# Kernel tuning notes

Measured on AMD Instinct MI355X. Metric: run time of the kernel, lower is better.

## Reference

```python
import jax, jax.numpy as jnp
import numpy as np

N_NODES = 50000


def gcn_conv(x, src, dst, W, b, n_nodes):
    """PyG GCNConv: add self-loops, sym-normalize, aggregate, linear.
    x' = D^{-1/2} (A + I) D^{-1/2} X W + b
    """
    loop = jnp.arange(n_nodes, dtype=src.dtype)
    s = jnp.concatenate([src, loop])  # [E + N]
    d = jnp.concatenate([dst, loop])
    h = x @ W  # [N, out]
    deg = jax.ops.segment_sum(jnp.ones_like(d, dtype=h.dtype), d, num_segments=n_nodes)
    dinv = jnp.where(deg > 0, jax.lax.rsqrt(deg), 0.0)
    norm = dinv[s] * dinv[d]  # [E + N]
    msg = h[s] * norm[:, None]  # gather + scale (edge-level, memory bound)
    out = jax.ops.segment_sum(msg, d, num_segments=n_nodes)
    return out + b


def setup_inputs() -> dict:
    key = jax.random.key(0)
    k1, k2, k3, k4 = jax.random.split(key, 4)
    n, e, d_in, d_hid, d_out = N_NODES, 800000, 128, 128, 64
    x = jax.random.normal(k1, (n, d_in), dtype=jnp.float32)
    edge_index = jax.random.randint(k2, (2, e), 0, n, dtype=jnp.int64)
    W1 = jax.random.normal(k3, (d_in, d_hid), dtype=jnp.float32) * (1.0 / np.sqrt(d_in))
    b1 = jnp.zeros((d_hid,), dtype=jnp.float32)
    W2 = jax.random.normal(k4, (d_hid, d_out), dtype=jnp.float32) * (1.0 / np.sqrt(d_hid))
    b2 = jnp.zeros((d_out,), dtype=jnp.float32)
    return {"x": x, "edge_index": edge_index, "W1": W1, "b1": b1, "W2": W2, "b2": b2}


def reference(x, edge_index, W1, b1, W2, b2):
    src, dst = edge_index[0], edge_index[1]
    h = gcn_conv(x, src, dst, W1, b1, N_NODES)
    h = jax.nn.relu(h)
    h = gcn_conv(h, src, dst, W2, b2, N_NODES)
    # edge-wise gather + dot product -> per-edge logits [E]
    logits = jnp.sum(h[src] * h[dst], axis=-1)
    return logits
```

## Files before the change

### kernel.cpp

```cpp
#include <hip/hip_runtime.h>
#include <hip/hip_bf16.h>


__global__ void cnt_k(const int* __restrict__ dst, int* __restrict__ cnt, int E) {
    int t = blockIdx.x * blockDim.x + threadIdx.x;
    int e = t * 4;
    if (e + 4 <= E) {
        int4 d4 = *reinterpret_cast<const int4*>(dst + e);
        atomicAdd(&cnt[d4.x], 1);
        atomicAdd(&cnt[d4.y], 1);
        atomicAdd(&cnt[d4.z], 1);
        atomicAdd(&cnt[d4.w], 1);
    } else {
        for (int i = e; i < E; i++) atomicAdd(&cnt[dst[i]], 1);
    }
}

__global__ void scan1_k(const int* __restrict__ cnt, int* __restrict__ incl,
                        int* __restrict__ bsum, int N) {
    __shared__ int sh[256];
    int i = blockIdx.x * 256 + threadIdx.x;
    int v = (i < N) ? cnt[i] : 0;
    sh[threadIdx.x] = v;
    __syncthreads();
#pragma unroll
    for (int off = 1; off < 256; off <<= 1) {
        int t = (threadIdx.x >= off) ? sh[threadIdx.x - off] : 0;
        __syncthreads();
        sh[threadIdx.x] += t;
        __syncthreads();
    }
    if (i < N) incl[i] = sh[threadIdx.x];
    if (threadIdx.x == 255) bsum[blockIdx.x] = sh[255];
}

__global__ __launch_bounds__(256) void scan23_k(const int* __restrict__ cnt,
                                                const int* __restrict__ incl,
                                                const int* __restrict__ bsum,
                                                int* __restrict__ rowptr,
                                                int* __restrict__ cursor,
                                                float* __restrict__ dinv,
                                                int N, int E, int NB) {
    __shared__ int sh[256];
    __shared__ int blockOff;
    int v = (threadIdx.x < NB) ? bsum[threadIdx.x] : 0;
    sh[threadIdx.x] = v;
    __syncthreads();
#pragma unroll
    for (int off = 1; off < 256; off <<= 1) {
        int t = (threadIdx.x >= off) ? sh[threadIdx.x - off] : 0;
        __syncthreads();
        sh[threadIdx.x] += t;
        __syncthreads();
    }
    if (threadIdx.x == blockIdx.x) blockOff = sh[threadIdx.x] - v;
    __syncthreads();
    int i = blockIdx.x * 256 + threadIdx.x;
    if (i < N) {
        int c = cnt[i];
        int excl = incl[i] - c + blockOff;
        rowptr[i] = excl;
        cursor[i] = excl;
        dinv[i] = rsqrtf(1.0f + (float)c);
    }
    if (i == 0) rowptr[N] = E;
}

__global__ __launch_bounds__(256) void gemm1_fill_k(const float* __restrict__ A,
                                                    const float* __restrict__ W,
                                                    const float* __restrict__ dscale,
                                                    float* __restrict__ Out, int M,
                                                    const int* __restrict__ src,
                                                    const int* __restrict__ dst,
                                                    int* __restrict__ cursor,
                                                    int2* __restrict__ col2, int E,
                                                    int gemmBlocks) {
    constexpr int K = 128, BM = 64, BK = 16, BN = 128, TN = 8;
    __shared__ float As[BK][BM + 4];
    __shared__ float Bs[BK][BN];

    if ((int)blockIdx.x >= gemmBlocks) {
        int t = ((int)blockIdx.x - gemmBlocks) * 256 + threadIdx.x;
        int e = t * 4;
        if (e + 4 <= E) {
            int4 s4 = *reinterpret_cast<const int4*>(src + e);
            int4 d4 = *reinterpret_cast<const int4*>(dst + e);
            int p0 = atomicAdd(&cursor[d4.x], 1);
            col2[p0] = make_int2(s4.x, e + 0);
            int p1 = atomicAdd(&cursor[d4.y], 1);
            col2[p1] = make_int2(s4.y, e + 1);
            int p2 = atomicAdd(&cursor[d4.z], 1);
            col2[p2] = make_int2(s4.z, e + 2);
            int p3 = atomicAdd(&cursor[d4.w], 1);
            col2[p3] = make_int2(s4.w, e + 3);
        } else {
            for (int i = e; i < E; i++) {
                int pos = atomicAdd(&cursor[dst[i]], 1);
                col2[pos] = make_int2(src[i], i);
            }
        }
        return;
    }

    const int tid = threadIdx.x;
    const int tx = tid & 15, ty = tid >> 4;
    const int row0 = blockIdx.x * BM;

    float acc[4][TN];
#pragma unroll
    for (int m = 0; m < 4; m++)
#pragma unroll
        for (int j = 0; j < TN; j++) acc[m][j] = 0.0f;

    const int ar = tid >> 2;
    const int ak = (tid & 3) * 4;

    for (int kt = 0; kt < K; kt += BK) {
        float4 av = make_float4(0.f, 0.f, 0.f, 0.f);
        int grow = row0 + ar;
        if (grow < M)
            av = *reinterpret_cast<const float4*>(A + (size_t)grow * K + kt + ak);
        As[ak + 0][ar] = av.x; As[ak + 1][ar] = av.y;
        As[ak + 2][ar] = av.z; As[ak + 3][ar] = av.w;

#pragma unroll
        for (int b = 0; b < 2; b++) {
            int f = b * 256 + tid;
            int brow = (f * 4) / BN;
            int bcol = (f * 4) % BN;
            float4 bv = *reinterpret_cast<const float4*>(W + (size_t)(kt + brow) * BN + bcol);
            *reinterpret_cast<float4*>(&Bs[brow][bcol]) = bv;
        }
        __syncthreads();

#pragma unroll
        for (int k = 0; k < BK; k++) {
            float4 a4 = *reinterpret_cast<const float4*>(&As[k][ty * 4]);
            float a[4] = {a4.x, a4.y, a4.z, a4.w};
            float bb[TN];
#pragma unroll
            for (int j4 = 0; j4 < TN / 4; j4++) {
                float4 b4 = *reinterpret_cast<const float4*>(&Bs[k][tx * TN + j4 * 4]);
                bb[j4 * 4 + 0] = b4.x; bb[j4 * 4 + 1] = b4.y;
                bb[j4 * 4 + 2] = b4.z; bb[j4 * 4 + 3] = b4.w;
            }
#pragma unroll
            for (int m = 0; m < 4; m++)
#pragma unroll
                for (int j = 0; j < TN; j++) acc[m][j] = fmaf(a[m], bb[j], acc[m][j]);
        }
        __syncthreads();
    }

#pragma unroll
    for (int m = 0; m < 4; m++) {
        int gr = row0 + ty * 4 + m;
        if (gr < M) {
            float dv = dscale[gr];
#pragma unroll
            for (int j4 = 0; j4 < TN / 4; j4++) {
                float4 o = make_float4(acc[m][j4 * 4 + 0] * dv, acc[m][j4 * 4 + 1] * dv,
                                       acc[m][j4 * 4 + 2] * dv, acc[m][j4 * 4 + 3] * dv);
                *reinterpret_cast<float4*>(Out + (size_t)gr * BN + tx * TN + j4 * 4) = o;
            }
        }
    }
}

__global__ __launch_bounds__(256) void gemm2_k(const float* __restrict__ A,
                                               const float* __restrict__ W,
                                               const float* __restrict__ dscale,
                                               float* __restrict__ Out, int M) {
    constexpr int K = 128, BM = 64, BK = 16, BN = 64, TN = 4;
    __shared__ float As[BK][BM + 4];
    __shared__ float Bs[BK][BN];

    const int tid = threadIdx.x;
    const int tx = tid & 15, ty = tid >> 4;
    const int row0 = blockIdx.x * BM;

    float acc[4][TN];
#pragma unroll
    for (int m = 0; m < 4; m++)
#pragma unroll
        for (int j = 0; j < TN; j++) acc[m][j] = 0.0f;

    const int ar = tid >> 2;
    const int ak = (tid & 3) * 4;

    for (int kt = 0; kt < K; kt += BK) {
        float4 av = make_float4(0.f, 0.f, 0.f, 0.f);
        int grow = row0 + ar;
        if (grow < M)
            av = *reinterpret_cast<const float4*>(A + (size_t)grow * K + kt + ak);
        av.x = fmaxf(av.x, 0.f); av.y = fmaxf(av.y, 0.f);
        av.z = fmaxf(av.z, 0.f); av.w = fmaxf(av.w, 0.f);
        As[ak + 0][ar] = av.x; As[ak + 1][ar] = av.y;
        As[ak + 2][ar] = av.z; As[ak + 3][ar] = av.w;

        {
            int f = tid;
            int brow = (f * 4) / BN;
            int bcol = (f * 4) % BN;
            float4 bv = *reinterpret_cast<const float4*>(W + (size_t)(kt + brow) * BN + bcol);
            *reinterpret_cast<float4*>(&Bs[brow][bcol]) = bv;
        }
        __syncthreads();

#pragma unroll
        for (int k = 0; k < BK; k++) {
            float4 a4 = *reinterpret_cast<const float4*>(&As[k][ty * 4]);
            float a[4] = {a4.x, a4.y, a4.z, a4.w};
            float4 b4 = *reinterpret_cast<const float4*>(&Bs[k][tx * TN]);
            float bb[TN] = {b4.x, b4.y, b4.z, b4.w};
#pragma unroll
            for (int m = 0; m < 4; m++)
#pragma unroll
                for (int j = 0; j < TN; j++) acc[m][j] = fmaf(a[m], bb[j], acc[m][j]);
        }
        __syncthreads();
    }

#pragma unroll
    for (int m = 0; m < 4; m++) {
        int gr = row0 + ty * 4 + m;
        if (gr < M) {
            float dv = dscale[gr];
            float4 o = make_float4(acc[m][0] * dv, acc[m][1] * dv,
                                   acc[m][2] * dv, acc[m][3] * dv);
            *reinterpret_cast<float4*>(Out + (size_t)gr * BN + tx * TN) = o;
        }
    }
}

__global__ __launch_bounds__(256) void pull128_k(const int* __restrict__ rowptr,
                                                 const int2* __restrict__ col2,
                                                 const float4* __restrict__ hs4,
                                                 const float* __restrict__ dinv,
                                                 const float4* __restrict__ bias4,
                                                 float4* __restrict__ out4, int N) {
    int wid = (int)((blockIdx.x * blockDim.x + threadIdx.x) >> 6);
    int nw = (int)((gridDim.x * blockDim.x) >> 6);
    int lane = threadIdx.x & 63;
    int q = lane & 31, slot = lane >> 5;

    for (int v = wid; v < N; v += nw) {
        int p0 = rowptr[v], p1 = rowptr[v + 1];

        float4 acc = make_float4(0.f, 0.f, 0.f, 0.f);
        if (slot == 0) acc = hs4[(size_t)v * 32 + q];

        int p = p0;
        for (; p + 8 <= p1; p += 8) {
            int ia = col2[p + slot].x, ib = col2[p + 2 + slot].x;
            int ic = col2[p + 4 + slot].x, id = col2[p + 6 + slot].x;
            float4 a = hs4[(size_t)ia * 32 + q];
            float4 b = hs4[(size_t)ib * 32 + q];
            float4 c = hs4[(size_t)ic * 32 + q];
            float4 d = hs4[(size_t)id * 32 + q];
            acc.x += (a.x + b.x) + (c.x + d.x);
            acc.y += (a.y + b.y) + (c.y + d.y);
            acc.z += (a.z + b.z) + (c.z + d.z);
            acc.w += (a.w + b.w) + (c.w + d.w);
        }
        for (; p + 2 <= p1; p += 2) {
            int ia = col2[p + slot].x;
            float4 a = hs4[(size_t)ia * 32 + q];
            acc.x += a.x; acc.y += a.y; acc.z += a.z; acc.w += a.w;
        }
        if (p < p1 && slot == 0) {
            float4 a = hs4[(size_t)col2[p].x * 32 + q];
            acc.x += a.x; acc.y += a.y; acc.z += a.z; acc.w += a.w;
        }

        acc.x += __shfl_xor(acc.x, 32);
        acc.y += __shfl_xor(acc.y, 32);
        acc.z += __shfl_xor(acc.z, 32);
        acc.w += __shfl_xor(acc.w, 32);

        if (slot == 0) {
            float dv = dinv[v];
            float4 bv = bias4[q];
            out4[(size_t)v * 32 + q] = make_float4(fmaf(acc.x, dv, bv.x), fmaf(acc.y, dv, bv.y),
                                                   fmaf(acc.z, dv, bv.z), fmaf(acc.w, dv, bv.w));
        }
    }
}

__global__ __launch_bounds__(256) void pull64_k(const int* __restrict__ rowptr,
                                                const int2* __restrict__ col2,
                                                const float4* __restrict__ hs4,
                                                const float* __restrict__ dinv,
                                                const float4* __restrict__ bias4,
                                                float4* __restrict__ out4, int N) {
    int wid = (int)((blockIdx.x * blockDim.x + threadIdx.x) >> 6);
    int nw = (int)((gridDim.x * blockDim.x) >> 6);
    int lane = threadIdx.x & 63;
    int q = lane & 15, slot = lane >> 4;

    for (int v = wid; v < N; v += nw) {
        int p0 = rowptr[v], p1 = rowptr[v + 1];

        float4 acc = make_float4(0.f, 0.f, 0.f, 0.f);
        if (slot == 0) acc = hs4[(size_t)v * 16 + q];

        int p = p0;
        for (; p + 8 <= p1; p += 8) {
            int ia = col2[p + slot].x, ib = col2[p + 4 + slot].x;
            float4 a = hs4[(size_t)ia * 16 + q];
            float4 b = hs4[(size_t)ib * 16 + q];
            acc.x += a.x + b.x; acc.y += a.y + b.y;
            acc.z += a.z + b.z; acc.w += a.w + b.w;
        }
        for (; p + 4 <= p1; p += 4) {
            float4 a = hs4[(size_t)col2[p + slot].x * 16 + q];
            acc.x += a.x; acc.y += a.y; acc.z += a.z; acc.w += a.w;
        }
        int rem = p1 - p;
        if (slot < rem) {
            float4 a = hs4[(size_t)col2[p + slot].x * 16 + q];
            acc.x += a.x; acc.y += a.y; acc.z += a.z; acc.w += a.w;
        }

#pragma unroll
        for (int off = 16; off <= 32; off <<= 1) {
            acc.x += __shfl_xor(acc.x, off);
            acc.y += __shfl_xor(acc.y, off);
            acc.z += __shfl_xor(acc.z, off);
            acc.w += __shfl_xor(acc.w, off);
        }

        if (slot == 0) {
            float dv = dinv[v];
            float4 bv = bias4[q];
            out4[(size_t)v * 16 + q] = make_float4(fmaf(acc.x, dv, bv.x), fmaf(acc.y, dv, bv.y),
                                                   fmaf(acc.z, dv, bv.z), fmaf(acc.w, dv, bv.w));
        }
    }
}

__global__ __launch_bounds__(256) void logits_csr_k(const int* __restrict__ rowptr,
                                                    const int2* __restrict__ col2,
                                                    const float4* __restrict__ h4,
                                                    float* __restrict__ out, int N) {
    int wid = (int)((blockIdx.x * blockDim.x + threadIdx.x) >> 6);
    int nw = (int)((gridDim.x * blockDim.x) >> 6);
    int lane = threadIdx.x & 63;
    int q = lane & 15, slot = lane >> 4;

    for (int v = wid; v < N; v += nw) {
        int p0 = rowptr[v], p1 = rowptr[v + 1];
        if (p0 == p1) continue;

        float4 rd = h4[(size_t)v * 16 + q];

        int p = p0;
        for (; p + 8 <= p1; p += 8) {
            int2 ca = col2[p + slot], cb = col2[p + 4 + slot];
            float4 ra = h4[(size_t)ca.x * 16 + q];
            float4 rb = h4[(size_t)cb.x * 16 + q];
            float t0 = rd.x * ra.x + rd.y * ra.y + rd.z * ra.z + rd.w * ra.w;
            float t1 = rd.x * rb.x + rd.y * rb.y + rd.z * rb.z + rd.w * rb.w;
#pragma unroll
            for (int off = 1; off < 16; off <<= 1) {
                t0 += __shfl_xor(t0, off);
                t1 += __shfl_xor(t1, off);
            }
            if (q == 0) { out[ca.y] = t0; out[cb.y] = t1; }
        }
        for (; p + 4 <= p1; p += 4) {
            int2 ca = col2[p + slot];
            float4 ra = h4[(size_t)ca.x * 16 + q];
            float t0 = rd.x * ra.x + rd.y * ra.y + rd.z * ra.z + rd.w * ra.w;
#pragma unroll
            for (int off = 1; off < 16; off <<= 1) t0 += __shfl_xor(t0, off);
            if (q == 0) out[ca.y] = t0;
        }
        int rem = p1 - p;
        if (slot < rem) {
            int2 ca = col2[p + slot];
            float4 ra = h4[(size_t)ca.x * 16 + q];
            float t0 = rd.x * ra.x + rd.y * ra.y + rd.z * ra.z + rd.w * ra.w;
#pragma unroll
            for (int off = 1; off < 16; off <<= 1) t0 += __shfl_xor(t0, off);
            if (q == 0) out[ca.y] = t0;
        }
    }
}

extern "C" void kernel_launch(void* const* d_in, const int* in_sizes, int n_in,
                              void* d_out, int out_size, void* d_ws, size_t ws_size,
                              hipStream_t stream) {
    const float* x  = (const float*)d_in[0];
    const int* ei   = (const int*)d_in[1];
    const float* W1 = (const float*)d_in[2];
    const float* b1 = (const float*)d_in[3];
    const float* W2 = (const float*)d_in[4];
    const float* b2 = (const float*)d_in[5];
    float* out = (float*)d_out;

    const int N = in_sizes[0] / 128;
    const int E = in_sizes[1] / 2;
    const int* src = ei;
    const int* dst = ei + E;

    float* ws   = (float*)d_ws;
    float* dinv = ws;
    float* bufA = ws + 50176;
    float* bufB = bufA + (size_t)N * 128;
    float* hs1  = bufA;
    float* agg1 = bufB;
    float* g2s  = bufA;
    float* agg2 = bufA + (size_t)N * 64;

    int* ibase  = (int*)(bufB + (size_t)N * 128);
    int* cnt    = ibase;
    int* incl   = cnt + N;
    int* rowptr = incl + N;
    int* cursor = rowptr + (N + 2);
    int* bsum   = cursor + N;
    int2* col2  = (int2*)(bsum + 256);

    const int B = 256;
    const int NB = (N + 255) / 256;
    const unsigned persBlocks = 2048;

    hipMemsetAsync(cnt, 0, (size_t)N * sizeof(int), stream);
    cnt_k<<<(E / 4 + B - 1) / B, B, 0, stream>>>(dst, cnt, E);
    scan1_k<<<NB, 256, 0, stream>>>(cnt, incl, bsum, N);
    scan23_k<<<NB, 256, 0, stream>>>(cnt, incl, bsum, rowptr, cursor, dinv, N, E, NB);

    {
        int gemmBlocks = (N + 63) / 64;
        int fillBlocks = (E / 4 + B - 1) / B;
        gemm1_fill_k<<<gemmBlocks + fillBlocks, 256, 0, stream>>>(
            x, W1, dinv, hs1, N, src, dst, cursor, col2, E, gemmBlocks);
    }

    pull128_k<<<persBlocks, 256, 0, stream>>>(rowptr, col2, (const float4*)hs1, dinv,
                                              (const float4*)b1, (float4*)agg1, N);

    gemm2_k<<<(N + 63) / 64, 256, 0, stream>>>(agg1, W2, dinv, g2s, N);
    pull64_k<<<persBlocks, 256, 0, stream>>>(rowptr, col2, (const float4*)g2s, dinv,
                                             (const float4*)b2, (float4*)agg2, N);

    logits_csr_k<<<persBlocks, 256, 0, stream>>>(rowptr, col2, (const float4*)agg2, out, N);
}
```

Baseline: 258.9 us.

## Load full A tile into LDS once and read W directly from global

Both dense GEMMs now share one templated body. It stages the whole 64x128 A tile into shared memory with coalesced float4 loads, padded to 132 columns, and uses a single barrier. The B operand (W) is no longer staged in LDS but read directly from global memory, relying on the cache since W is small and shared by every block. This removes the per-K-step barriers and transposed scalar LDS stores. In exchange the A tile uses more shared memory, which may lower occupancy, and every thread issues repeated global loads for W.

Measured after the change: 298.3 us. +15.2%, slower.

```diff
diff --git a/kernel.cpp b/kernel.cpp
--- a/kernel.cpp
+++ b/kernel.cpp
@@ -66,6 +66,80 @@
     if (i == 0) rowptr[N] = E;
 }
 
+template <int BN, bool RELU>
+__device__ __forceinline__ void gemm_body(const float* __restrict__ A,
+                                          const float* __restrict__ W,
+                                          const float* __restrict__ dscale,
+                                          float* __restrict__ Out, int M,
+                                          float (*As)[132], int row0) {
+    constexpr int K = 128;
+    constexpr int TN = BN / 16;
+    const int tid = threadIdx.x;
+
+#pragma unroll
+    for (int s = 0; s < 8; s++) {
+        int flat = s * 256 + tid;
+        int r = flat >> 5;
+        int c4 = (flat & 31) << 2;
+        float4 av = make_float4(0.f, 0.f, 0.f, 0.f);
+        int gr = row0 + r;
+        if (gr < M)
+            av = *reinterpret_cast<const float4*>(A + (size_t)gr * K + c4);
+        if (RELU) {
+            av.x = fmaxf(av.x, 0.f); av.y = fmaxf(av.y, 0.f);
+            av.z = fmaxf(av.z, 0.f); av.w = fmaxf(av.w, 0.f);
+        }
+        *reinterpret_cast<float4*>(&As[r][c4]) = av;
+    }
+    __syncthreads();
+
+    const int tx = tid & 15, ty = tid >> 4;
+    float acc[4][TN];
+#pragma unroll
+    for (int m = 0; m < 4; m++)
+#pragma unroll
+        for (int n = 0; n < TN; n++) acc[m][n] = 0.0f;
+
+    const float* Wp = W + tx * TN;
+
+#pragma unroll 4
+    for (int k = 0; k < K; k += 4) {
+        float a[4][4];
+#pragma unroll
+        for (int m = 0; m < 4; m++)
+            *reinterpret_cast<float4*>(a[m]) =
+                *reinterpret_cast<const float4*>(&As[ty * 4 + m][k]);
+#pragma unroll
+        for (int kk = 0; kk < 4; kk++) {
+#pragma unroll
+            for (int j4 = 0; j4 < TN / 4; j4++) {
+                float4 bv = *reinterpret_cast<const float4*>(Wp + (size_t)(k + kk) * BN + j4 * 4);
+#pragma unroll
+                for (int m = 0; m < 4; m++) {
+                    acc[m][j4 * 4 + 0] = fmaf(a[m][kk], bv.x, acc[m][j4 * 4 + 0]);
+                    acc[m][j4 * 4 + 1] = fmaf(a[m][kk], bv.y, acc[m][j4 * 4 + 1]);
+                    acc[m][j4 * 4 + 2] = fmaf(a[m][kk], bv.z, acc[m][j4 * 4 + 2]);
+                    acc[m][j4 * 4 + 3] = fmaf(a[m][kk], bv.w, acc[m][j4 * 4 + 3]);
+                }
+            }
+        }
+    }
+
+#pragma unroll
+    for (int m = 0; m < 4; m++) {
+        int gr = row0 + ty * 4 + m;
+        if (gr < M) {
+            float dv = dscale[gr];
+#pragma unroll
+            for (int j4 = 0; j4 < TN / 4; j4++) {
+                float4 o = make_float4(acc[m][j4 * 4 + 0] * dv, acc[m][j4 * 4 + 1] * dv,
+                                       acc[m][j4 * 4 + 2] * dv, acc[m][j4 * 4 + 3] * dv);
+                *reinterpret_cast<float4*>(Out + (size_t)gr * BN + tx * TN + j4 * 4) = o;
+            }
+        }
+    }
+}
+
 __global__ __launch_bounds__(256) void gemm1_fill_k(const float* __restrict__ A,
                                                     const float* __restrict__ W,
                                                     const float* __restrict__ dscale,
@@ -75,10 +149,7 @@
                                                     int* __restrict__ cursor,
                                                     int2* __restrict__ col2, int E,
                                                     int gemmBlocks) {
-    constexpr int K = 128, BM = 64, BK = 16, BN = 128, TN = 8;
-    __shared__ float As[BK][BM + 4];
-    __shared__ float Bs[BK][BN];
-
+    __shared__ float As[64][132];
     if ((int)blockIdx.x >= gemmBlocks) {
         int t = ((int)blockIdx.x - gemmBlocks) * 256 + threadIdx.x;
         int e = t * 4;
@@ -101,136 +172,15 @@
         }
         return;
     }
-
-    const int tid = threadIdx.x;
-    const int tx = tid & 15, ty = tid >> 4;
-    const int row0 = blockIdx.x * BM;
-
-    float acc[4][TN];
-#pragma unroll
-    for (int m = 0; m < 4; m++)
-#pragma unroll
-        for (int j = 0; j < TN; j++) acc[m][j] = 0.0f;
-
-    const int ar = tid >> 2;
-    const int ak = (tid & 3) * 4;
-
-    for (int kt = 0; kt < K; kt += BK) {
-        float4 av = make_float4(0.f, 0.f, 0.f, 0.f);
-        int grow = row0 + ar;
-        if (grow < M)
-            av = *reinterpret_cast<const float4*>(A + (size_t)grow * K + kt + ak);
-        As[ak + 0][ar] = av.x; As[ak + 1][ar] = av.y;
-        As[ak + 2][ar] = av.z; As[ak + 3][ar] = av.w;
-
-#pragma unroll
-        for (int b = 0; b < 2; b++) {
-            int f = b * 256 + tid;
-            int brow = (f * 4) / BN;
-            int bcol = (f * 4) % BN;
-            float4 bv = *reinterpret_cast<const float4*>(W + (size_t)(kt + brow) * BN + bcol);
-            *reinterpret_cast<float4*>(&Bs[brow][bcol]) = bv;
-        }
-        __syncthreads();
-
-#pragma unroll
-        for (int k = 0; k < BK; k++) {
-            float4 a4 = *reinterpret_cast<const float4*>(&As[k][ty * 4]);
-            float a[4] = {a4.x, a4.y, a4.z, a4.w};
-            float bb[TN];
-#pragma unroll
-            for (int j4 = 0; j4 < TN / 4; j4++) {
-                float4 b4 = *reinterpret_cast<const float4*>(&Bs[k][tx * TN + j4 * 4]);
-                bb[j4 * 4 + 0] = b4.x; bb[j4 * 4 + 1] = b4.y;
-                bb[j4 * 4 + 2] = b4.z; bb[j4 * 4 + 3] = b4.w;
-            }
-#pragma unroll
-            for (int m = 0; m < 4; m++)
-#pragma unroll
-                for (int j = 0; j < TN; j++) acc[m][j] = fmaf(a[m], bb[j], acc[m][j]);
-        }
-        __syncthreads();
-    }
-
-#pragma unroll
-    for (int m = 0; m < 4; m++) {
-        int gr = row0 + ty * 4 + m;
-        if (gr < M) {
-            float dv = dscale[gr];
-#pragma unroll
-            for (int j4 = 0; j4 < TN / 4; j4++) {
-                float4 o = make_float4(acc[m][j4 * 4 + 0] * dv, acc[m][j4 * 4 + 1] * dv,
-                                       acc[m][j4 * 4 + 2] * dv, acc[m][j4 * 4 + 3] * dv);
-                *reinterpret_cast<float4*>(Out + (size_t)gr * BN + tx * TN + j4 * 4) = o;
-            }
-        }
-    }
+    gemm_body<128, false>(A, W, dscale, Out, M, As, (int)blockIdx.x * 64);
 }
 
 __global__ __launch_bounds__(256) void gemm2_k(const float* __restrict__ A,
                                                const float* __restrict__ W,
                                                const float* __restrict__ dscale,
                                                float* __restrict__ Out, int M) {
-    constexpr int K = 128, BM = 64, BK = 16, BN = 64, TN = 4;
-    __shared__ float As[BK][BM + 4];
-    __shared__ float Bs[BK][BN];
-
-    const int tid = threadIdx.x;
-    const int tx = tid & 15, ty = tid >> 4;
-    const int row0 = blockIdx.x * BM;
-
-    float acc[4][TN];
-#pragma unroll
-    for (int m = 0; m < 4; m++)
-#pragma unroll
-        for (int j = 0; j < TN; j++) acc[m][j] = 0.0f;
-
-    const int ar = tid >> 2;
-    const int ak = (tid & 3) * 4;
-
-    for (int kt = 0; kt < K; kt += BK) {
-        float4 av = make_float4(0.f, 0.f, 0.f, 0.f);
-        int grow = row0 + ar;
-        if (grow < M)
-            av = *reinterpret_cast<const float4*>(A + (size_t)grow * K + kt + ak);
-        av.x = fmaxf(av.x, 0.f); av.y = fmaxf(av.y, 0.f);
-        av.z = fmaxf(av.z, 0.f); av.w = fmaxf(av.w, 0.f);
-        As[ak + 0][ar] = av.x; As[ak + 1][ar] = av.y;
-        As[ak + 2][ar] = av.z; As[ak + 3][ar] = av.w;
-
-        {
-            int f = tid;
-            int brow = (f * 4) / BN;
-            int bcol = (f * 4) % BN;
-            float4 bv = *reinterpret_cast<const float4*>(W + (size_t)(kt + brow) * BN + bcol);
-            *reinterpret_cast<float4*>(&Bs[brow][bcol]) = bv;
-        }
-        __syncthreads();
-
-#pragma unroll
-        for (int k = 0; k < BK; k++) {
-            float4 a4 = *reinterpret_cast<const float4*>(&As[k][ty * 4]);
-            float a[4] = {a4.x, a4.y, a4.z, a4.w};
-            float4 b4 = *reinterpret_cast<const float4*>(&Bs[k][tx * TN]);
-            float bb[TN] = {b4.x, b4.y, b4.z, b4.w};
-#pragma unroll
-            for (int m = 0; m < 4; m++)
-#pragma unroll
-                for (int j = 0; j < TN; j++) acc[m][j] = fmaf(a[m], bb[j], acc[m][j]);
-        }
-        __syncthreads();
-    }
-
-#pragma unroll
-    for (int m = 0; m < 4; m++) {
-        int gr = row0 + ty * 4 + m;
-        if (gr < M) {
-            float dv = dscale[gr];
-            float4 o = make_float4(acc[m][0] * dv, acc[m][1] * dv,
-                                   acc[m][2] * dv, acc[m][3] * dv);
-            *reinterpret_cast<float4*>(Out + (size_t)gr * BN + tx * TN) = o;
-        }
-    }
+    __shared__ float As[64][132];
+    gemm_body<64, true>(A, W, dscale, Out, M, As, (int)blockIdx.x * 64);
 }
 
 __global__ __launch_bounds__(256) void pull128_k(const int* __restrict__ rowptr,
```
